# Kernel tuning notes

Measured on AMD Instinct MI355X. Metric: run time of the kernel, lower is better.

The kernel has to match this reference:

```python
import jax, jax.numpy as jnp
import numpy as np

C, C_H, N_HEAD = 8, 1, 8


def setup_inputs() -> dict:
    key = jax.random.key(0)
    ks = jax.random.split(key, 8)
    B, S, I, c = 1, 4096, 1024, C
    hd = C_H * N_HEAD
    m = jax.random.normal(ks[0], (B, S, I, c), dtype=jnp.float32)
    mask = jnp.ones((B, S, I), dtype=jnp.float32)
    return {
        "m": m,
        "mask": mask,
        "ln_w": jnp.ones((c,), jnp.float32),
        "ln_b": jnp.zeros((c,), jnp.float32),
        "wq": jax.random.normal(ks[1], (hd, c), jnp.float32) * 0.1,
        "wk": jax.random.normal(ks[2], (C_H, c), jnp.float32) * 0.1,
        "wv": jax.random.normal(ks[3], (C_H, c), jnp.float32) * 0.1,
        "wg": jax.random.normal(ks[4], (hd, c), jnp.float32) * 0.1,
        "bg": jnp.zeros((hd,), jnp.float32),
        "wo": jax.random.normal(ks[5], (c, hd), jnp.float32) * 0.1,
        "bo": jnp.zeros((c,), jnp.float32),
    }


def _layer_norm(x, w, b, eps=1e-5):
    mu = jnp.mean(x, axis=-1, keepdims=True)
    var = jnp.mean(jnp.square(x - mu), axis=-1, keepdims=True)
    return (x - mu) * jax.lax.rsqrt(var + eps) * w + b


def reference(m, mask, ln_w, ln_b, wq, wk, wv, wg, bg, wo, bo):
    h, c_h = N_HEAD, C_H
    # transpose so attention runs over the sequence (column) axis s
    mt = jnp.swapaxes(m, -2, -3)        # (B, i, s, c)
    mk = jnp.swapaxes(mask, -1, -2)     # (B, i, s)
    mn = _layer_norm(mt, ln_w, ln_b)    # (B, i, s, c)
    # masked mean-pooled query over s
    q = jnp.sum(mn * mk[..., None], axis=-2) / (jnp.sum(mk, axis=-1)[..., None] + 1e-5)  # (B,i,c)
    q = (q @ wq.T) * (c_h ** -0.5)                      # (B, i, h*c_h)
    q = q.reshape(*q.shape[:-1], h, c_h)                # (B, i, h, c_h)
    k = mn @ wk.T                                       # (B, i, s, c_h)
    v = mn @ wv.T                                       # (B, i, s, c_h)
    g = jax.nn.sigmoid(mn @ wg.T + bg)                  # (B, i, s, h*c_h)
    g = g.reshape(*g.shape[:-1], h, c_h)                # (B, i, s, h, c_h)
    bias = (1e9 * (mk - 1.0))[..., None, :]             # (B, i, 1, s)
    a = jnp.einsum('bihd,bisd->bihs', q, k) + bias      # (B, i, h, s)
    a = jax.nn.softmax(a, axis=-1)
    o = jnp.einsum('bihs,bisd->bihd', a, v)             # (B, i, h, c_h)
    o = o[..., None, :, :] * g                          # (B, i, s, h, c_h)
    o = o.reshape(*o.shape[:-2], h * c_h)               # (B, i, s, h*c_h)
    o = o @ wo.T + bo                                   # (B, i, s, c)
    return jnp.swapaxes(o, -2, -3)                      # (B, s, i, c)
```

## Files before the change

### kernel.cpp

```cpp
#include <hip/hip_runtime.h>

#define SS 4096
#define II 1024

#define WOFF  0
#define FLAGW 254
#define QSOFF 256
#define MSOFF 8448
#define OAOFF 9472
#define KOFF  17664
#define VOFF  4211968
#define BOFF  8406272

using u16 = unsigned short;

__device__ __forceinline__ float b2f(unsigned int u) {
    union { unsigned int i; float f; } t; t.i = u << 16; return t.f;
}
__device__ __forceinline__ u16 f2b(float f) {
    union { float f; unsigned int i; } t; t.f = f;
    unsigned int x = t.i;
    return (u16)((x + 0x7fffu + ((x >> 16) & 1u)) >> 16);
}
__device__ __forceinline__ void unpack8(const uint4 p, float x[8]) {
    x[0] = b2f(p.x & 0xffffu); x[1] = b2f(p.x >> 16);
    x[2] = b2f(p.y & 0xffffu); x[3] = b2f(p.y >> 16);
    x[4] = b2f(p.z & 0xffffu); x[5] = b2f(p.z >> 16);
    x[6] = b2f(p.w & 0xffffu); x[7] = b2f(p.w >> 16);
}
__device__ __forceinline__ void load8(const void* m, size_t idx, int bf, float x[8]) {
    if (bf) {
        const uint4 p = ((const uint4*)m)[idx];
        unpack8(p, x);
    } else {
        const float4 a = ((const float4*)m)[idx * 2];
        const float4 b = ((const float4*)m)[idx * 2 + 1];
        x[0]=a.x; x[1]=a.y; x[2]=a.z; x[3]=a.w;
        x[4]=b.x; x[5]=b.y; x[6]=b.z; x[7]=b.w;
    }
}
__device__ __forceinline__ float load1(const void* p, size_t idx, int bf) {
    return bf ? b2f((unsigned int)((const u16*)p)[idx]) : ((const float*)p)[idx];
}

__global__ void wconv(const void* lnw, const void* lnb, const void* wq,
                      const void* wk,  const void* wv,  const void* wg,
                      const void* bg,  const void* wo,  const void* bo,
                      float* __restrict__ W) {
    const float probe = ((const float*)lnw)[0];
    const int bf = (fabsf(probe - 1.0f) > 1e-6f) ? 1 : 0;
    const int t = threadIdx.x;
    if (t < 8)  W[t]       = load1(lnw, t, bf);
    if (t < 8)  W[8 + t]   = load1(lnb, t, bf);
    if (t < 64) W[16 + t]  = load1(wq,  t, bf);
    if (t < 8)  W[80 + t]  = load1(wk,  t, bf);
    if (t < 8)  W[88 + t]  = load1(wv,  t, bf);
    if (t < 64) W[96 + t]  = load1(wg,  t, bf);
    if (t < 8)  W[160 + t] = load1(bg,  t, bf);
    if (t < 64) W[168 + t] = load1(wo,  t, bf);
    if (t < 8)  W[232 + t] = load1(bo,  t, bf);
    if (t == 0) W[FLAGW]   = (float)bf;
}

__global__ __launch_bounds__(256) void stage1(const void* __restrict__ m,
                                              const void* __restrict__ mask,
                                              const float* __restrict__ W,
                                              float* __restrict__ ws) {
    __shared__ float tile[64 * 65];
    __shared__ float qred[4 * 64 * 8];
    __shared__ float mred[4 * 64];
    const int tx = threadIdx.x, ty = threadIdx.y;
    const int i  = blockIdx.x * 64 + tx;
    const int s0 = blockIdx.y * 64;
    const int bf = (int)W[FLAGW];

    float lnw[8], lnb[8], wk[8], wv[8];
#pragma unroll
    for (int j = 0; j < 8; j++) {
        lnw[j] = W[j]; lnb[j] = W[8 + j]; wk[j] = W[80 + j]; wv[j] = W[88 + j];
    }

    float kreg[16], vreg[16], breg[16];
    float qs[8] = {0.f,0.f,0.f,0.f,0.f,0.f,0.f,0.f};
    float ms = 0.f;
#pragma unroll
    for (int t = 0; t < 16; t++) {
        const int s = s0 + ty + 4 * t;
        float x[8];
        load8(m, (size_t)s * II + i, bf, x);
        float mu = 0.f;
#pragma unroll
        for (int j = 0; j < 8; j++) mu += x[j];
        mu *= 0.125f;
        float var = 0.f;
#pragma unroll
        for (int j = 0; j < 8; j++) { float d = x[j] - mu; var += d * d; }
        var *= 0.125f;
        const float rs = 1.0f / sqrtf(var + 1e-5f);
        const float mk = load1(mask, (size_t)s * II + i, bf);
        float kv = 0.f, vv = 0.f;
#pragma unroll
        for (int j = 0; j < 8; j++) {
            const float n = (x[j] - mu) * rs * lnw[j] + lnb[j];
            kv += wk[j] * n;
            vv += wv[j] * n;
            qs[j] += n * mk;
        }
        ms += mk;
        kreg[t] = kv; vreg[t] = vv; breg[t] = 1e9f * (mk - 1.0f);
    }

#pragma unroll
    for (int j = 0; j < 8; j++) qred[(ty * 64 + tx) * 8 + j] = qs[j];
    mred[ty * 64 + tx] = ms;
    __syncthreads();
    if (ty == 0) {
#pragma unroll
        for (int j = 0; j < 8; j++) {
            float v = qred[tx * 8 + j] + qred[(64 + tx) * 8 + j] +
                      qred[(128 + tx) * 8 + j] + qred[(192 + tx) * 8 + j];
            atomicAdd(&ws[QSOFF + (size_t)i * 8 + j], v);
        }
        float v = mred[tx] + mred[64 + tx] + mred[128 + tx] + mred[192 + tx];
        atomicAdd(&ws[MSOFF + i], v);
    }

#pragma unroll
    for (int a = 0; a < 3; a++) {
        __syncthreads();
#pragma unroll
        for (int t = 0; t < 16; t++)
            tile[(ty + 4 * t) * 65 + tx] = (a == 0) ? kreg[t] : ((a == 1) ? vreg[t] : breg[t]);
        __syncthreads();
        float* dst = ws + ((a == 0) ? (size_t)KOFF : ((a == 1) ? (size_t)VOFF : (size_t)BOFF));
#pragma unroll
        for (int t = 0; t < 16; t++) {
            const int il = ty + 4 * t;
            dst[(size_t)(blockIdx.x * 64 + il) * SS + s0 + tx] = tile[tx * 65 + il];
        }
    }
}

__global__ __launch_bounds__(256) void attn_reduce(float* __restrict__ ws) {
    __shared__ __attribute__((aligned(16))) float sk[SS];
    __shared__ __attribute__((aligned(16))) float sv[SS];
    __shared__ __attribute__((aligned(16))) float sb[SS];
    __shared__ float red[12];
    const int i = blockIdx.x;
    const int tid = threadIdx.x;
    const int lane = tid & 63, wid = tid >> 6;

    const float4* kp = (const float4*)(ws + KOFF + (size_t)i * SS);
    const float4* vp = (const float4*)(ws + VOFF + (size_t)i * SS);
    const float4* bp = (const float4*)(ws + BOFF + (size_t)i * SS);
#pragma unroll
    for (int t = 0; t < 4; t++) {
        int idx = t * 256 + tid;
        ((float4*)sk)[idx] = kp[idx];
        ((float4*)sv)[idx] = vp[idx];
        ((float4*)sb)[idx] = bp[idx];
    }

    const float inv = 1.0f / (ws[MSOFF + i] + 1e-5f);
    float qp[8];
#pragma unroll
    for (int j = 0; j < 8; j++) qp[j] = ws[QSOFF + (size_t)i * 8 + j] * inv;
    float qh[8];
#pragma unroll
    for (int h = 0; h < 8; h++) {
        float a = 0.f;
#pragma unroll
        for (int j = 0; j < 8; j++) a += ws[16 + h * 8 + j] * qp[j];
        qh[h] = a;
    }
    __syncthreads();

    float oat[8];
    for (int h = 0; h < 8; h++) {
        const float q = qh[h];
        float av[16];
        float lm = -3.4e38f;
#pragma unroll
        for (int t = 0; t < 16; t++) {
            int s = t * 256 + tid;
            av[t] = q * sk[s] + sb[s];
            lm = fmaxf(lm, av[t]);
        }
#pragma unroll
        for (int off = 32; off; off >>= 1) lm = fmaxf(lm, __shfl_xor(lm, off, 64));
        if (lane == 0) red[wid] = lm;
        __syncthreads();
        const float M = fmaxf(fmaxf(red[0], red[1]), fmaxf(red[2], red[3]));
        float lz = 0.f, ln = 0.f;
#pragma unroll
        for (int t = 0; t < 16; t++) {
            float e = expf(av[t] - M);
            lz += e;
            ln += e * sv[t * 256 + tid];
        }
#pragma unroll
        for (int off = 32; off; off >>= 1) {
            lz += __shfl_xor(lz, off, 64);
            ln += __shfl_xor(ln, off, 64);
        }
        if (lane == 0) { red[4 + wid] = lz; red[8 + wid] = ln; }
        __syncthreads();
        const float Z = red[4] + red[5] + red[6] + red[7];
        const float N = red[8] + red[9] + red[10] + red[11];
        oat[h] = N / Z;
        __syncthreads();
    }
    if (tid < 8) ws[OAOFF + (size_t)i * 8 + tid] = oat[tid];
}

__global__ __launch_bounds__(256) void outk(const void* __restrict__ m,
                                            const float* __restrict__ W,
                                            const float* __restrict__ oatt,
                                            void* __restrict__ out) {
    const size_t idx = (size_t)blockIdx.x * 256 + threadIdx.x;
    const int i = (int)(idx & (II - 1));
    const int bf = (int)W[FLAGW];
    float x[8];
    load8(m, idx, bf, x);
    float mu = 0.f;
#pragma unroll
    for (int j = 0; j < 8; j++) mu += x[j];
    mu *= 0.125f;
    float var = 0.f;
#pragma unroll
    for (int j = 0; j < 8; j++) { float d = x[j] - mu; var += d * d; }
    var *= 0.125f;
    const float rs = 1.0f / sqrtf(var + 1e-5f);
    float n[8];
#pragma unroll
    for (int j = 0; j < 8; j++) n[j] = (x[j] - mu) * rs * W[j] + W[8 + j];

    float o[8];
#pragma unroll
    for (int h = 0; h < 8; h++) {
        float z = W[160 + h];
#pragma unroll
        for (int j = 0; j < 8; j++) z += W[96 + h * 8 + j] * n[j];
        const float g = 1.0f / (1.0f + expf(-z));
        o[h] = oatt[(size_t)i * 8 + h] * g;
    }

    float y[8];
#pragma unroll
    for (int cc = 0; cc < 8; cc++) {
        float acc = W[232 + cc];
#pragma unroll
        for (int h = 0; h < 8; h++) acc += W[168 + cc * 8 + h] * o[h];
        y[cc] = acc;
    }
    if (bf) {
        u16 r[8];
#pragma unroll
        for (int cc = 0; cc < 8; cc++) r[cc] = f2b(y[cc]);
        uint4 q;
        q.x = (unsigned)r[0] | ((unsigned)r[1] << 16);
        q.y = (unsigned)r[2] | ((unsigned)r[3] << 16);
        q.z = (unsigned)r[4] | ((unsigned)r[5] << 16);
        q.w = (unsigned)r[6] | ((unsigned)r[7] << 16);
        ((uint4*)out)[idx] = q;
    } else {
        float4 a, b;
        a.x=y[0]; a.y=y[1]; a.z=y[2]; a.w=y[3];
        b.x=y[4]; b.y=y[5]; b.z=y[6]; b.w=y[7];
        ((float4*)out)[idx * 2]     = a;
        ((float4*)out)[idx * 2 + 1] = b;
    }
}

extern "C" void kernel_launch(void* const* d_in, const int* in_sizes, int n_in,
                              void* d_out, int out_size, void* d_ws, size_t ws_size,
                              hipStream_t stream) {
    const void* m    = d_in[0];
    const void* mask = d_in[1];
    const void* lnw  = d_in[2];
    const void* lnb  = d_in[3];
    const void* wq   = d_in[4];
    const void* wk   = d_in[5];
    const void* wv   = d_in[6];
    const void* wg   = d_in[7];
    const void* bg   = d_in[8];
    const void* wo   = d_in[9];
    const void* bo   = d_in[10];
    float* ws = (float*)d_ws;

    wconv<<<1, 64, 0, stream>>>(lnw, lnb, wq, wk, wv, wg, bg, wo, bo, ws);
    hipMemsetAsync(ws + QSOFF, 0, (size_t)(OAOFF - QSOFF) * sizeof(float), stream);

    dim3 b1(64, 4), g1(II / 64, SS / 64);
    stage1<<<g1, b1, 0, stream>>>(m, mask, ws, ws);

    attn_reduce<<<II, 256, 0, stream>>>(ws);

    outk<<<(SS * II) / 256, 256, 0, stream>>>(m, ws, ws + OAOFF, d_out);
}
```

Before: 348.3 us.

## Fuse memset into weight kernel, retile stage1, batch heads in attention reduce

The workspace memset is folded into a multi-block wconv launch, which removes one stream operation. stage1 now uses 512-thread blocks over 32-row sequence tiles, writes results directly into a shared tile, reduces q with shared atomics and stores K/V/bias with float4 writes. attn_reduce processes all 8 heads in a single pass, cutting the per-head syncs from 24 to 2 at the cost of more registers. Fast __expf replaces expf in the softmax and the gate sigmoid, which trades a little accuracy for speed.

```diff
diff --git a/kernel.cpp b/kernel.cpp
--- a/kernel.cpp
+++ b/kernel.cpp
@@ -3,7 +3,6 @@
 #define SS 4096
 #define II 1024
 
-#define WOFF  0
 #define FLAGW 254
 #define QSOFF 256
 #define MSOFF 8448
@@ -50,42 +49,52 @@
     const float probe = ((const float*)lnw)[0];
     const int bf = (fabsf(probe - 1.0f) > 1e-6f) ? 1 : 0;
     const int t = threadIdx.x;
-    if (t < 8)  W[t]       = load1(lnw, t, bf);
-    if (t < 8)  W[8 + t]   = load1(lnb, t, bf);
-    if (t < 64) W[16 + t]  = load1(wq,  t, bf);
-    if (t < 8)  W[80 + t]  = load1(wk,  t, bf);
-    if (t < 8)  W[88 + t]  = load1(wv,  t, bf);
-    if (t < 64) W[96 + t]  = load1(wg,  t, bf);
-    if (t < 8)  W[160 + t] = load1(bg,  t, bf);
-    if (t < 64) W[168 + t] = load1(wo,  t, bf);
-    if (t < 8)  W[232 + t] = load1(bo,  t, bf);
-    if (t == 0) W[FLAGW]   = (float)bf;
-}
-
-__global__ __launch_bounds__(256) void stage1(const void* __restrict__ m,
-                                              const void* __restrict__ mask,
-                                              const float* __restrict__ W,
-                                              float* __restrict__ ws) {
-    __shared__ float tile[64 * 65];
-    __shared__ float qred[4 * 64 * 8];
-    __shared__ float mred[4 * 64];
+    if (blockIdx.x == 0) {
+        if (t < 8)  W[t]       = load1(lnw, t, bf);
+        if (t < 8)  W[8 + t]   = load1(lnb, t, bf);
+        if (t < 64) W[16 + t]  = load1(wq,  t, bf);
+        if (t < 8)  W[80 + t]  = load1(wk,  t, bf);
+        if (t < 8)  W[88 + t]  = load1(wv,  t, bf);
+        if (t < 64) W[96 + t]  = load1(wg,  t, bf);
+        if (t < 8)  W[160 + t] = load1(bg,  t, bf);
+        if (t < 64) W[168 + t] = load1(wo,  t, bf);
+        if (t < 8)  W[232 + t] = load1(bo,  t, bf);
+        if (t == 0) W[FLAGW]   = (float)bf;
+    }
+    const int idx = blockIdx.x * 256 + t;
+    if (idx < OAOFF - QSOFF) W[QSOFF + idx] = 0.f;
+}
+
+__global__ __launch_bounds__(512, 6) void stage1(const void* __restrict__ m,
+                                                 const void* __restrict__ mask,
+                                                 const float* __restrict__ W,
+                                                 float* __restrict__ ws) {
+    __shared__ float tile[3][32][65];
+    __shared__ float qacc[64][9];
+    __shared__ float macc[64];
     const int tx = threadIdx.x, ty = threadIdx.y;
+    const int tid = ty * 64 + tx;
     const int i  = blockIdx.x * 64 + tx;
-    const int s0 = blockIdx.y * 64;
+    const int s0 = blockIdx.y * 32;
     const int bf = (int)W[FLAGW];
 
-    float lnw[8], lnb[8], wk[8], wv[8];
+    if (tid < 64) macc[tid] = 0.f;
+    ((float*)qacc)[tid] = 0.f;
+    if (tid < 64) ((float*)qacc)[512 + tid] = 0.f;
+    __syncthreads();
+
+    float lnw[8], lnb[8], wkr[8], wvr[8];
 #pragma unroll
     for (int j = 0; j < 8; j++) {
-        lnw[j] = W[j]; lnb[j] = W[8 + j]; wk[j] = W[80 + j]; wv[j] = W[88 + j];
-    }
-
-    float kreg[16], vreg[16], breg[16];
+        lnw[j] = W[j]; lnb[j] = W[8 + j]; wkr[j] = W[80 + j]; wvr[j] = W[88 + j];
+    }
+
     float qs[8] = {0.f,0.f,0.f,0.f,0.f,0.f,0.f,0.f};
     float ms = 0.f;
 #pragma unroll
-    for (int t = 0; t < 16; t++) {
-        const int s = s0 + ty + 4 * t;
+    for (int t = 0; t < 4; t++) {
+        const int sl = ty + 8 * t;
+        const int s  = s0 + sl;
         float x[8];
         load8(m, (size_t)s * II + i, bf, x);
         float mu = 0.f;
@@ -102,42 +111,38 @@
 #pragma unroll
         for (int j = 0; j < 8; j++) {
             const float n = (x[j] - mu) * rs * lnw[j] + lnb[j];
-            kv += wk[j] * n;
-            vv += wv[j] * n;
+            kv += wkr[j] * n;
+            vv += wvr[j] * n;
             qs[j] += n * mk;
         }
         ms += mk;
-        kreg[t] = kv; vreg[t] = vv; breg[t] = 1e9f * (mk - 1.0f);
-    }
-
-#pragma unroll
-    for (int j = 0; j < 8; j++) qred[(ty * 64 + tx) * 8 + j] = qs[j];
-    mred[ty * 64 + tx] = ms;
-    __syncthreads();
+        tile[0][sl][tx] = kv;
+        tile[1][sl][tx] = vv;
+        tile[2][sl][tx] = 1e9f * (mk - 1.0f);
+    }
+
+#pragma unroll
+    for (int j = 0; j < 8; j++) atomicAdd(&qacc[tx][j], qs[j]);
+    atomicAdd(&macc[tx], ms);
+    __syncthreads();
+
     if (ty == 0) {
 #pragma unroll
-        for (int j = 0; j < 8; j++) {
-            float v = qred[tx * 8 + j] + qred[(64 + tx) * 8 + j] +
-                      qred[(128 + tx) * 8 + j] + qred[(192 + tx) * 8 + j];
-            atomicAdd(&ws[QSOFF + (size_t)i * 8 + j], v);
-        }
-        float v = mred[tx] + mred[64 + tx] + mred[128 + tx] + mred[192 + tx];
-        atomicAdd(&ws[MSOFF + i], v);
-    }
-
+        for (int j = 0; j < 8; j++) atomicAdd(&ws[QSOFF + (size_t)i * 8 + j], qacc[tx][j]);
+        atomicAdd(&ws[MSOFF + i], macc[tx]);
+    }
+
+    const int iL = tid >> 3;
+    const int s4 = (tid & 7) * 4;
 #pragma unroll
     for (int a = 0; a < 3; a++) {
-        __syncthreads();
-#pragma unroll
-        for (int t = 0; t < 16; t++)
-            tile[(ty + 4 * t) * 65 + tx] = (a == 0) ? kreg[t] : ((a == 1) ? vreg[t] : breg[t]);
-        __syncthreads();
+        float4 w;
+        w.x = tile[a][s4    ][iL];
+        w.y = tile[a][s4 + 1][iL];
+        w.z = tile[a][s4 + 2][iL];
+        w.w = tile[a][s4 + 3][iL];
         float* dst = ws + ((a == 0) ? (size_t)KOFF : ((a == 1) ? (size_t)VOFF : (size_t)BOFF));
-#pragma unroll
-        for (int t = 0; t < 16; t++) {
-            const int il = ty + 4 * t;
-            dst[(size_t)(blockIdx.x * 64 + il) * SS + s0 + tx] = tile[tx * 65 + il];
-        }
+        *(float4*)(dst + (size_t)(blockIdx.x * 64 + iL) * SS + s0 + s4) = w;
     }
 }
 
@@ -145,7 +150,7 @@
     __shared__ __attribute__((aligned(16))) float sk[SS];
     __shared__ __attribute__((aligned(16))) float sv[SS];
     __shared__ __attribute__((aligned(16))) float sb[SS];
-    __shared__ float red[12];
+    __shared__ float redm[8][4], redz[8][4], redn[8][4];
     const int i = blockIdx.x;
     const int tid = threadIdx.x;
     const int lane = tid & 63, wid = tid >> 6;
@@ -175,42 +180,62 @@
     }
     __syncthreads();
 
-    float oat[8];
+    float lm[8];
+#pragma unroll
+    for (int h = 0; h < 8; h++) lm[h] = -3.4e38f;
+#pragma unroll
+    for (int t = 0; t < 16; t++) {
+        const int s = t * 256 + tid;
+        const float k = sk[s], b = sb[s];
+#pragma unroll
+        for (int h = 0; h < 8; h++) lm[h] = fmaxf(lm[h], qh[h] * k + b);
+    }
+#pragma unroll
     for (int h = 0; h < 8; h++) {
-        const float q = qh[h];
-        float av[16];
-        float lm = -3.4e38f;
-#pragma unroll
-        for (int t = 0; t < 16; t++) {
-            int s = t * 256 + tid;
-            av[t] = q * sk[s] + sb[s];
-            lm = fmaxf(lm, av[t]);
+#pragma unroll
+        for (int off = 32; off; off >>= 1) lm[h] = fmaxf(lm[h], __shfl_xor(lm[h], off, 64));
+    }
+    if (lane == 0) {
+#pragma unroll
+        for (int h = 0; h < 8; h++) redm[h][wid] = lm[h];
+    }
+    __syncthreads();
+    float M[8];
+#pragma unroll
+    for (int h = 0; h < 8; h++)
+        M[h] = fmaxf(fmaxf(redm[h][0], redm[h][1]), fmaxf(redm[h][2], redm[h][3]));
+
+    float lz[8] = {0,0,0,0,0,0,0,0}, ln[8] = {0,0,0,0,0,0,0,0};
+#pragma unroll
+    for (int t = 0; t < 16; t++) {
+        const int s = t * 256 + tid;
+        const float k = sk[s], b = sb[s], v = sv[s];
+#pragma unroll
+        for (int h = 0; h < 8; h++) {
+            const float e = __expf(qh[h] * k + b - M[h]);
+            lz[h] += e;
+            ln[h] += e * v;
         }
-#pragma unroll
-        for (int off = 32; off; off >>= 1) lm = fmaxf(lm, __shfl_xor(lm, off, 64));
-        if (lane == 0) red[wid] = lm;
-        __syncthreads();
-        const float M = fmaxf(fmaxf(red[0], red[1]), fmaxf(red[2], red[3]));
-        float lz = 0.f, ln = 0.f;
-#pragma unroll
-        for (int t = 0; t < 16; t++) {
-            float e = expf(av[t] - M);
-            lz += e;
-            ln += e * sv[t * 256 + tid];
+    }
+#pragma unroll
+    for (int h = 0; h < 8; h++) {
+#pragma unroll
+        for (int off = 32; off; off >>= 1) {
+            lz[h] += __shfl_xor(lz[h], off, 64);
+            ln[h] += __shfl_xor(ln[h], off, 64);
         }
-#pragma unroll
-        for (int off = 32; off; off >>= 1) {
-            lz += __shfl_xor(lz, off, 64);
-            ln += __shfl_xor(ln, off, 64);
-        }
-        if (lane == 0) { red[4 + wid] = lz; red[8 + wid] = ln; }
-        __syncthreads();
-        const float Z = red[4] + red[5] + red[6] + red[7];
-        const float N = red[8] + red[9] + red[10] + red[11];
-        oat[h] = N / Z;
-        __syncthreads();
-    }
-    if (tid < 8) ws[OAOFF + (size_t)i * 8 + tid] = oat[tid];
+    }
+    if (lane == 0) {
+#pragma unroll
+        for (int h = 0; h < 8; h++) { redz[h][wid] = lz[h]; redn[h][wid] = ln[h]; }
+    }
+    __syncthreads();
+    if (tid < 8) {
+        const int h = tid;
+        const float Z = redz[h][0] + redz[h][1] + redz[h][2] + redz[h][3];
+        const float N = redn[h][0] + redn[h][1] + redn[h][2] + redn[h][3];
+        ws[OAOFF + (size_t)i * 8 + h] = N / Z;
+    }
 }
 
 __global__ __launch_bounds__(256) void outk(const void* __restrict__ m,
@@ -241,7 +266,7 @@
         float z = W[160 + h];
 #pragma unroll
         for (int j = 0; j < 8; j++) z += W[96 + h * 8 + j] * n[j];
-        const float g = 1.0f / (1.0f + expf(-z));
+        const float g = 1.0f / (1.0f + __expf(-z));
         o[h] = oatt[(size_t)i * 8 + h] * g;
     }
 
@@ -275,26 +300,15 @@
 extern "C" void kernel_launch(void* const* d_in, const int* in_sizes, int n_in,
                               void* d_out, int out_size, void* d_ws, size_t ws_size,
                               hipStream_t stream) {
-    const void* m    = d_in[0];
-    const void* mask = d_in[1];
-    const void* lnw  = d_in[2];
-    const void* lnb  = d_in[3];
-    const void* wq   = d_in[4];
-    const void* wk   = d_in[5];
-    const void* wv   = d_in[6];
-    const void* wg   = d_in[7];
-    const void* bg   = d_in[8];
-    const void* wo   = d_in[9];
-    const void* bo   = d_in[10];
     float* ws = (float*)d_ws;
 
-    wconv<<<1, 64, 0, stream>>>(lnw, lnb, wq, wk, wv, wg, bg, wo, bo, ws);
-    hipMemsetAsync(ws + QSOFF, 0, (size_t)(OAOFF - QSOFF) * sizeof(float), stream);
-
-    dim3 b1(64, 4), g1(II / 64, SS / 64);
-    stage1<<<g1, b1, 0, stream>>>(m, mask, ws, ws);
+    wconv<<<37, 256, 0, stream>>>(d_in[2], d_in[3], d_in[4], d_in[5], d_in[6],
+                                  d_in[7], d_in[8], d_in[9], d_in[10], ws);
+
+    dim3 b1(64, 8), g1(II / 64, SS / 32);
+    stage1<<<g1, b1, 0, stream>>>(d_in[0], d_in[1], ws, ws);
 
     attn_reduce<<<II, 256, 0, stream>>>(ws);
 
-    outk<<<(SS * II) / 256, 256, 0, stream>>>(m, ws, ws + OAOFF, d_out);
-}
+    outk<<<(SS * II) / 256, 256, 0, stream>>>(d_in[0], ws, ws + OAOFF, d_out);
+}
```

Result: slower. 355.7 us (+2.1%).
